# Kernel tuning notes

Hardware: AMD Instinct MI355X
Metric: run time of the kernel (lower is better)

## Reference

```python
import jax, jax.numpy as jnp
import numpy as np

N = 50000
E = 600000
D_IN = 128
D_HID = 128
D_OUT = 40
EPS = 1e-5


def glorot(key, shape):
    lim = float(np.sqrt(6.0 / (shape[0] + shape[1])))
    return jax.random.uniform(key, shape, jnp.float32, -lim, lim)


def setup_inputs() -> dict:
    key = jax.random.key(0)
    ks = jax.random.split(key, 8)
    return {
        "node_feat": jax.random.normal(ks[0], (N, D_IN), jnp.float32),
        "edge_src": jax.random.randint(ks[1], (E,), 0, N, jnp.int32),
        "edge_dst": jax.random.randint(ks[2], (E,), 0, N, jnp.int32),
        # input BatchNorm (bn_1)
        "bn0_g": jnp.ones((D_IN,), jnp.float32),
        "bn0_b": jnp.zeros((D_IN,), jnp.float32),
        # conv 1 (in -> hidden) + its BN
        "W1": glorot(ks[3], (D_IN, D_HID)),
        "b1": jnp.zeros((D_HID,), jnp.float32),
        "bn1_g": jnp.ones((D_HID,), jnp.float32),
        "bn1_b": jnp.zeros((D_HID,), jnp.float32),
        # conv 2 (hidden -> hidden) + its BN
        "W2": glorot(ks[4], (D_HID, D_HID)),
        "b2": jnp.zeros((D_HID,), jnp.float32),
        "bn2_g": jnp.ones((D_HID,), jnp.float32),
        "bn2_b": jnp.zeros((D_HID,), jnp.float32),
        # final projection
        "Wf": glorot(ks[5], (D_HID, D_OUT)),
        "bf": jnp.zeros((D_OUT,), jnp.float32),
    }


def batchnorm(x, gamma, beta):
    # BatchNorm1d over nodes (batch-stat / training-mode normalization)
    mu = jnp.mean(x, axis=0)
    var = jnp.mean(jnp.square(x - mu), axis=0)
    return gamma * (x - mu) * jax.lax.rsqrt(var + EPS) + beta


def gcn_conv(x, W, b, src, dst, norm, self_norm):
    # GCNConv: D^{-1/2}(A+I)D^{-1/2} X W + b
    h = x @ W  # [N, d_out]
    agg = jax.ops.segment_sum(h[src] * norm[:, None], dst, num_segments=N)
    agg = agg + h * self_norm[:, None]  # self-loop contribution
    return agg + b


def reference(node_feat, edge_src, edge_dst, bn0_g, bn0_b, W1, b1, bn1_g, bn1_b,
              W2, b2, bn2_g, bn2_b, Wf, bf):
    # degree with self-loops: deg_i = |{e : dst(e)=i}| + 1
    deg = jnp.ones((N,), jnp.float32).at[edge_dst].add(1.0)
    dinv = jax.lax.rsqrt(deg)
    norm = dinv[edge_src] * dinv[edge_dst]  # [E]
    self_norm = dinv * dinv                 # [N]

    x = batchnorm(node_feat, bn0_g, bn0_b)

    x = gcn_conv(x, W1, b1, edge_src, edge_dst, norm, self_norm)
    x = batchnorm(x, bn1_g, bn1_b)
    x = jax.nn.relu(x)  # dropout is identity in eval mode

    x = gcn_conv(x, W2, b2, edge_src, edge_dst, norm, self_norm)
    x = batchnorm(x, bn2_g, bn2_b)
    x = jax.nn.relu(x)

    return x @ Wf + bf  # [N, D_OUT]
```

## Files before the change

### kernel.cpp

```cpp
#include <hip/hip_runtime.h>
#include <cstdint>
#include <cstddef>


#define CS_BLOCKS 512

typedef short  s8v __attribute__((ext_vector_type(8)));
typedef ushort u8v __attribute__((ext_vector_type(8)));
typedef float  f4v __attribute__((ext_vector_type(4)));

__device__ inline ushort f2bf(float f) {
    uint u = __float_as_uint(f);
    return (ushort)((u + 0x7fffu + ((u >> 16) & 1u)) >> 16);
}
__device__ inline float bf2f(ushort u) {
    return __uint_as_float((uint)u << 16);
}
__device__ inline float2 bf2f2(uint u) {
    float2 r;
    r.x = __uint_as_float(u << 16);
    r.y = __uint_as_float(u & 0xffff0000u);
    return r;
}

__global__ __launch_bounds__(256) void k_prolog(const float* __restrict__ X,
                                                int n, float* __restrict__ part,
                                                const float* __restrict__ W1,
                                                const float* __restrict__ W2,
                                                ushort* __restrict__ Wswz,
                                                int* __restrict__ cnt) {
    const int bid = blockIdx.x;
    if (bid < CS_BLOCKS) {
        __shared__ float ls[8 * 128];
        __shared__ float lq[8 * 128];
        const int c4    = threadIdx.x & 31;
        const int rslot = threadIdx.x >> 5;
        float4 s4 = make_float4(0.f, 0.f, 0.f, 0.f);
        float4 q4 = make_float4(0.f, 0.f, 0.f, 0.f);
        const float4* X4 = (const float4*)X;
        for (int r = bid * 8 + rslot; r < n; r += CS_BLOCKS * 8) {
            float4 v = X4[(size_t)r * 32 + c4];
            s4.x += v.x; s4.y += v.y; s4.z += v.z; s4.w += v.w;
            q4.x = fmaf(v.x, v.x, q4.x); q4.y = fmaf(v.y, v.y, q4.y);
            q4.z = fmaf(v.z, v.z, q4.z); q4.w = fmaf(v.w, v.w, q4.w);
        }
        *(float4*)&ls[rslot * 128 + c4 * 4] = s4;
        *(float4*)&lq[rslot * 128 + c4 * 4] = q4;
        __syncthreads();
        float t = 0.f;
        if (threadIdx.x < 128) {
            int c = threadIdx.x;
            #pragma unroll
            for (int k = 0; k < 8; ++k) t += ls[k * 128 + c];
        } else {
            int c = threadIdx.x - 128;
            #pragma unroll
            for (int k = 0; k < 8; ++k) t += lq[k * 128 + c];
        }
        part[bid * 256 + threadIdx.x] = t;
    } else if (bid < CS_BLOCKS + 16) {
        const int wb = bid - CS_BLOCKS;
        const float* W = (wb < 8) ? W1 : W2;
        ushort* out = Wswz + (wb < 8 ? 0 : 16384);
        int t  = (wb & 7) * 256 + threadIdx.x;
        int l  = t & 63;
        int fi = t >> 6;
        int ks = fi & 3, ct = fi >> 2;
        int c  = ct * 16 + (l & 15);
        int k0 = ks * 32 + ((l >> 4) << 3);
        ushort o[8];
        #pragma unroll
        for (int j = 0; j < 8; ++j)
            o[j] = f2bf(W[(size_t)(k0 + j) * 128 + c]);
        ushort4* dst = (ushort4*)(out + (size_t)t * 8);
        dst[0] = make_ushort4(o[0], o[1], o[2], o[3]);
        dst[1] = make_ushort4(o[4], o[5], o[6], o[7]);
    } else {
        const int zb = bid - CS_BLOCKS - 16;
        const int nv = n >> 2;
        int4* c4p = (int4*)cnt;
        const int4 z = make_int4(0, 0, 0, 0);
        for (int i = zb * 256 + threadIdx.x; i < nv; i += 64 * 256)
            c4p[i] = z;
        int i = (nv << 2) + zb * 256 + threadIdx.x;
        if (i < n) cnt[i] = 0;
    }
}

__device__ inline void redA_body(const float* __restrict__ part,
                                 float* __restrict__ part2,
                                 int nrows, int b) {
    const int c = threadIdx.x;
    const int per = (nrows + 63) >> 6;
    const int r0 = b * per;
    const int r1 = min(r0 + per, nrows);
    float t0 = 0.f, t1 = 0.f;
    int r = r0;
    for (; r + 2 <= r1; r += 2) {
        t0 += part[(size_t)r * 256 + c];
        t1 += part[(size_t)(r + 1) * 256 + c];
    }
    if (r < r1) t0 += part[(size_t)r * 256 + c];
    part2[b * 256 + c] = t0 + t1;
}

__global__ __launch_bounds__(256) void k_redA(const float* __restrict__ part,
                                              float* __restrict__ part2,
                                              int nrows) {
    redA_body(part, part2, nrows, blockIdx.x);
}

__device__ inline void bn_inblock(const float* __restrict__ part2,
                                  const float* __restrict__ g,
                                  const float* __restrict__ be,
                                  float invn, float* __restrict__ tmp,
                                  float* __restrict__ abuf,
                                  float* __restrict__ bbuf) {
    const int tid = threadIdx.x;
    float t = 0.f;
    #pragma unroll 8
    for (int r = 0; r < 64; ++r) t += part2[r * 256 + tid];
    tmp[tid] = t;
    __syncthreads();
    if (tid < 128) {
        float mu  = tmp[tid] * invn;
        float var = tmp[tid + 128] * invn - mu * mu;
        float av  = g[tid] * rsqrtf(var + 1e-5f);
        abuf[tid] = av;
        bbuf[tid] = be[tid] - mu * av;
    }
    __syncthreads();
}

__global__ __launch_bounds__(256) void k_count(const int* __restrict__ dst, int e,
                                               int* __restrict__ cnt,
                                               int* __restrict__ rank) {
    int i = blockIdx.x * 256 + threadIdx.x;
    if (i < e) rank[i] = atomicAdd(&cnt[dst[i]], 1);
}

__global__ __launch_bounds__(1024) void k_scanA(const int* __restrict__ cnt, int n,
                                                int* __restrict__ rs, int* __restrict__ bsum) {
    __shared__ int tmp[1024];
    int t = threadIdx.x;
    int i = blockIdx.x * 1024 + t;
    int v = (i < n) ? cnt[i] : 0;
    tmp[t] = v;
    __syncthreads();
    for (int off = 1; off < 1024; off <<= 1) {
        int x = (t >= off) ? tmp[t - off] : 0;
        __syncthreads();
        tmp[t] += x;
        __syncthreads();
    }
    if (i < n) rs[i] = tmp[t] - v;
    if (t == 1023) bsum[blockIdx.x] = tmp[t];
}

__global__ __launch_bounds__(256) void k_scanC(int* __restrict__ rs,
                                               const int* __restrict__ bsum,
                                               const int* __restrict__ cnt,
                                               float* __restrict__ dinv,
                                               int n, int e) {
    __shared__ int base;
    int chunk = (int)(blockIdx.x >> 2);
    if (threadIdx.x == 0) {
        int s = 0;
        for (int c = 0; c < chunk; ++c) s += bsum[c];
        base = s;
    }
    __syncthreads();
    int i = blockIdx.x * 256 + threadIdx.x;
    if (i < n) {
        rs[i] += base;
        dinv[i] = rsqrtf((float)(cnt[i] + 1));
    }
    if (blockIdx.x == 0 && threadIdx.x == 0) rs[n] = e;
}

__global__ __launch_bounds__(256) void k_fill(const int* __restrict__ src,
                                              const int* __restrict__ dst, int e,
                                              const int* __restrict__ rs,
                                              const int* __restrict__ rank,
                                              const float* __restrict__ dinv,
                                              int2* __restrict__ ep,
                                              const float* __restrict__ part,
                                              float* __restrict__ part2,
                                              int fillBlocks) {
    const int bid = blockIdx.x;
    if (bid < fillBlocks) {
        int i = bid * 256 + threadIdx.x;
        if (i < e) {
            int d = dst[i], s = src[i];
            int p = rs[d] + rank[i];
            float nm = dinv[s] * dinv[d];
            ep[p] = make_int2(s, __float_as_int(nm));
        }
    } else {
        redA_body(part, part2, CS_BLOCKS, bid - fillBlocks);
    }
}

template<int BF16IN>
__global__ __launch_bounds__(256) void k_gemm_mfma(const void* __restrict__ Xv,
                                                   const ushort* __restrict__ Wswz,
                                                   const float* __restrict__ part2,
                                                   const float* __restrict__ g,
                                                   const float* __restrict__ be,
                                                   float invn, int relu,
                                                   ushort* __restrict__ H, int n) {
    __shared__ ushort xb[64 * 128];
    __shared__ float tmp[256];
    __shared__ float abuf[128], bbuf[128];
    const int tid  = threadIdx.x;
    const int row0 = blockIdx.x * 64;

    bn_inblock(part2, g, be, invn, tmp, abuf, bbuf);

    if (BF16IN) {
        const ushort* X = (const ushort*)Xv;
        for (int i = tid; i < 64 * 16; i += 256) {
            int r = i >> 4, c8 = i & 15;
            int gr = row0 + r;
            u8v raw = {0, 0, 0, 0, 0, 0, 0, 0};
            if (gr < n) raw = *(const u8v*)(X + (size_t)gr * 128 + c8 * 8);
            ushort o[8];
            #pragma unroll
            for (int j = 0; j < 8; ++j) {
                float f = fmaf(bf2f(raw[j]), abuf[c8 * 8 + j], bbuf[c8 * 8 + j]);
                if (relu) f = fmaxf(f, 0.f);
                o[j] = f2bf(f);
            }
            int off = (r * 256 + c8 * 16) ^ ((r & 7) << 4);
            ushort4* dst = (ushort4*)((char*)xb + off);
            dst[0] = make_ushort4(o[0], o[1], o[2], o[3]);
            dst[1] = make_ushort4(o[4], o[5], o[6], o[7]);
        }
    } else {
        const float* X = (const float*)Xv;
        for (int i = tid; i < 64 * 32; i += 256) {
            int r = i >> 5, c4 = i & 31;
            int gr = row0 + r;
            float4 v = make_float4(0.f, 0.f, 0.f, 0.f);
            if (gr < n) v = ((const float4*)X)[(size_t)gr * 32 + c4];
            float4 a4 = *(const float4*)&abuf[c4 * 4];
            float4 b4 = *(const float4*)&bbuf[c4 * 4];
            v.x = fmaf(v.x, a4.x, b4.x);
            v.y = fmaf(v.y, a4.y, b4.y);
            v.z = fmaf(v.z, a4.z, b4.z);
            v.w = fmaf(v.w, a4.w, b4.w);
            if (relu) {
                v.x = fmaxf(v.x, 0.f); v.y = fmaxf(v.y, 0.f);
                v.z = fmaxf(v.z, 0.f); v.w = fmaxf(v.w, 0.f);
            }
            ushort4 pk = make_ushort4(f2bf(v.x), f2bf(v.y), f2bf(v.z), f2bf(v.w));
            int off = (r * 256 + c4 * 8) ^ ((r & 7) << 4);
            *(ushort4*)((char*)xb + off) = pk;
        }
    }
    __syncthreads();

    const int wv = tid >> 6;
    const int l  = tid & 63;
    const int arow = wv * 16 + (l & 15);

    s8v afr[4];
    #pragma unroll
    for (int ks = 0; ks < 4; ++ks) {
        int off = (arow * 256 + ks * 64 + ((l >> 4) << 4)) ^ ((arow & 7) << 4);
        afr[ks] = *(const s8v*)((const char*)xb + off);
    }

    const s8v* wf = (const s8v*)Wswz;
    f4v acc[8];
    #pragma unroll
    for (int ct = 0; ct < 8; ++ct) {
        f4v c = {0.f, 0.f, 0.f, 0.f};
        #pragma unroll
        for (int ks = 0; ks < 4; ++ks) {
            s8v bb = wf[(ct * 4 + ks) * 64 + l];
            c = __builtin_amdgcn_mfma_f32_16x16x32_bf16(afr[ks], bb, c, 0, 0, 0);
        }
        acc[ct] = c;
    }

    const int rbase = row0 + wv * 16 + ((l >> 4) << 2);
    const int cidx  = l & 15;
    #pragma unroll
    for (int r = 0; r < 4; ++r) {
        int gr = rbase + r;
        if (gr < n) {
            #pragma unroll
            for (int ct = 0; ct < 8; ++ct)
                H[(size_t)gr * 128 + ct * 16 + cidx] = f2bf(acc[ct][r]);
        }
    }
}

template<int NP>
__device__ inline void quad_batch(const ushort* __restrict__ H,
                                  const int2* __restrict__ ep,
                                  int i, int q, int sl, float* __restrict__ a) {
    int2 p[NP]; uint4 v[NP];
    #pragma unroll
    for (int k = 0; k < NP; ++k) p[k] = ep[i + 4 * k + q];
    #pragma unroll
    for (int k = 0; k < NP; ++k)
        v[k] = ((const uint4*)(H + (size_t)p[k].x * 128))[sl];
    #pragma unroll
    for (int k = 0; k < NP; ++k) {
        float w = __int_as_float(p[k].y);
        float2 f0 = bf2f2(v[k].x), f1 = bf2f2(v[k].y);
        float2 f2 = bf2f2(v[k].z), f3 = bf2f2(v[k].w);
        a[0] = fmaf(w, f0.x, a[0]); a[1] = fmaf(w, f0.y, a[1]);
        a[2] = fmaf(w, f1.x, a[2]); a[3] = fmaf(w, f1.y, a[3]);
        a[4] = fmaf(w, f2.x, a[4]); a[5] = fmaf(w, f2.y, a[5]);
        a[6] = fmaf(w, f3.x, a[6]); a[7] = fmaf(w, f3.y, a[7]);
    }
}

__global__ __launch_bounds__(256) void k_aggregate(const ushort* __restrict__ H,
                                                   const int* __restrict__ rs,
                                                   const int2* __restrict__ ep,
                                                   const float* __restrict__ dinv,
                                                   ushort* __restrict__ AGG,
                                                   float* __restrict__ part, int n) {
    __shared__ float red[4][128];
    __shared__ float redq[4][128];
    const int wv   = threadIdx.x >> 6;
    const int lane = threadIdx.x & 63;
    const int q    = lane >> 4;
    const int sl   = lane & 15;
    const int node = blockIdx.x * 4 + wv;
    float a[8] = {0.f, 0.f, 0.f, 0.f, 0.f, 0.f, 0.f, 0.f};

    if (node < n) {
        if (q == 0) {
            float sn = dinv[node]; sn *= sn;
            uint4 sv = ((const uint4*)(H + (size_t)node * 128))[sl];
            float2 f0 = bf2f2(sv.x), f1 = bf2f2(sv.y);
            float2 f2 = bf2f2(sv.z), f3 = bf2f2(sv.w);
            a[0] = sn * f0.x; a[1] = sn * f0.y;
            a[2] = sn * f1.x; a[3] = sn * f1.y;
            a[4] = sn * f2.x; a[5] = sn * f2.y;
            a[6] = sn * f3.x; a[7] = sn * f3.y;
        }
        int i  = rs[node];
        int i1 = rs[node + 1];
        for (; i + 16 <= i1; i += 16) quad_batch<4>(H, ep, i, q, sl, a);
        if (i + 8 <= i1) { quad_batch<2>(H, ep, i, q, sl, a); i += 8; }
        if (i + 4 <= i1) { quad_batch<1>(H, ep, i, q, sl, a); i += 4; }
        if (i < i1) {
            int idx = min(i + q, i1 - 1);
            int2 p = ep[idx];
            float w = (i + q < i1) ? __int_as_float(p.y) : 0.f;
            uint4 v = ((const uint4*)(H + (size_t)p.x * 128))[sl];
            float2 f0 = bf2f2(v.x), f1 = bf2f2(v.y);
            float2 f2 = bf2f2(v.z), f3 = bf2f2(v.w);
            a[0] = fmaf(w, f0.x, a[0]); a[1] = fmaf(w, f0.y, a[1]);
            a[2] = fmaf(w, f1.x, a[2]); a[3] = fmaf(w, f1.y, a[3]);
            a[4] = fmaf(w, f2.x, a[4]); a[5] = fmaf(w, f2.y, a[5]);
            a[6] = fmaf(w, f3.x, a[6]); a[7] = fmaf(w, f3.y, a[7]);
        }
        #pragma unroll
        for (int j = 0; j < 8; ++j) {
            a[j] += __shfl_xor(a[j], 16);
            a[j] += __shfl_xor(a[j], 32);
        }
        if (q == 0) {
            u8v o;
            #pragma unroll
            for (int j = 0; j < 8; ++j) o[j] = f2bf(a[j]);
            *(u8v*)(AGG + (size_t)node * 128 + sl * 8) = o;
        }
    }

    if (q == 0) {
        *(float4*)&red[wv][8 * sl]      = make_float4(a[0], a[1], a[2], a[3]);
        *(float4*)&red[wv][8 * sl + 4]  = make_float4(a[4], a[5], a[6], a[7]);
        *(float4*)&redq[wv][8 * sl]     = make_float4(a[0] * a[0], a[1] * a[1],
                                                      a[2] * a[2], a[3] * a[3]);
        *(float4*)&redq[wv][8 * sl + 4] = make_float4(a[4] * a[4], a[5] * a[5],
                                                      a[6] * a[6], a[7] * a[7]);
    }
    __syncthreads();
    const int t = threadIdx.x;
    if (t < 128)
        part[(size_t)blockIdx.x * 256 + t] =
            red[0][t] + red[1][t] + red[2][t] + red[3][t];
    else {
        int c = t - 128;
        part[(size_t)blockIdx.x * 256 + t] =
            redq[0][c] + redq[1][c] + redq[2][c] + redq[3][c];
    }
}

__global__ __launch_bounds__(256) void k_gemm_out(const ushort* __restrict__ X,
                                                  const float* __restrict__ Wf,
                                                  const float* __restrict__ bfv,
                                                  const float* __restrict__ part2,
                                                  const float* __restrict__ g,
                                                  const float* __restrict__ be,
                                                  float invn,
                                                  float* __restrict__ OUT, int n) {
    __shared__ float xl[32 * 132];
    __shared__ float wt[40 * 132];
    __shared__ float tmp[256];
    __shared__ float abuf[128], bbuf[128];
    const int tid = threadIdx.x;

    bn_inblock(part2, g, be, invn, tmp, abuf, bbuf);

    for (int i = tid; i < 128 * 40; i += 256) {
        int c = i / 40;
        int j = i - c * 40;
        wt[j * 132 + c] = Wf[i];
    }
    const int row0 = blockIdx.x * 32;
    for (int i = tid; i < 32 * 16; i += 256) {
        int r = i >> 4, c8 = i & 15;
        int gr = row0 + r;
        u8v raw = {0, 0, 0, 0, 0, 0, 0, 0};
        if (gr < n) raw = *(const u8v*)(X + (size_t)gr * 128 + c8 * 8);
        float o[8];
        #pragma unroll
        for (int j = 0; j < 8; ++j)
            o[j] = fmaxf(fmaf(bf2f(raw[j]), abuf[c8 * 8 + j],
                              bbuf[c8 * 8 + j]), 0.f);
        *(float4*)&xl[r * 132 + c8 * 8]     = make_float4(o[0], o[1], o[2], o[3]);
        *(float4*)&xl[r * 132 + c8 * 8 + 4] = make_float4(o[4], o[5], o[6], o[7]);
    }
    __syncthreads();

    const int rg = tid >> 3;
    const int cg = tid & 7;
    const int j0 = cg * 5;
    float acc[5] = {0.f, 0.f, 0.f, 0.f, 0.f};
    for (int c = 0; c < 128; c += 4) {
        float4 xv = *(const float4*)&xl[rg * 132 + c];
        #pragma unroll
        for (int j = 0; j < 5; ++j) {
            float4 wv = *(const float4*)&wt[(j0 + j) * 132 + c];
            acc[j] = fmaf(xv.x, wv.x, acc[j]);
            acc[j] = fmaf(xv.y, wv.y, acc[j]);
            acc[j] = fmaf(xv.z, wv.z, acc[j]);
            acc[j] = fmaf(xv.w, wv.w, acc[j]);
        }
    }
    int gr = row0 + rg;
    if (gr < n) {
        #pragma unroll
        for (int j = 0; j < 5; ++j)
            OUT[(size_t)gr * 40 + j0 + j] = acc[j] + bfv[j0 + j];
    }
}

extern "C" void kernel_launch(void* const* d_in, const int* in_sizes, int n_in,
                              void* d_out, int out_size, void* d_ws, size_t ws_size,
                              hipStream_t stream) {
    const float* X0      = (const float*)d_in[0];
    const int*   edgesrc = (const int*)d_in[1];
    const int*   edgedst = (const int*)d_in[2];
    const float* bn0g = (const float*)d_in[3];
    const float* bn0b = (const float*)d_in[4];
    const float* W1   = (const float*)d_in[5];
    const float* bn1g = (const float*)d_in[7];
    const float* bn1b = (const float*)d_in[8];
    const float* W2   = (const float*)d_in[9];
    const float* bn2g = (const float*)d_in[11];
    const float* bn2b = (const float*)d_in[12];
    const float* Wf   = (const float*)d_in[13];
    const float* bfv  = (const float*)d_in[14];

    const int n = in_sizes[0] / 128;
    const int e = in_sizes[1];
    float* OUT = (float*)d_out;

    const int aggBlocks = (n + 3) / 4;

    ushort* H    = (ushort*)d_ws;
    ushort* AGGb = H + (size_t)n * 128;
    float*  dinv = (float*)(AGGb + (size_t)n * 128);
    int2*   ep   = (int2*)(dinv + n);
    ushort* Wswz = (ushort*)(ep + e);
    int*    cnt  = (int*)(Wswz + 2 * 16384);
    int*    rs   = cnt + n;
    int*    rank = rs + n + 1;
    int*    bsum = rank + e;
    float*  part = (float*)(bsum + 64);
    float* part2 = part + (size_t)aggBlocks * 256;

    const float invn = 1.f / (float)n;
    const int nb = (n + 1023) / 1024;
    const int fillBlocks = (e + 255) / 256;

    k_prolog<<<CS_BLOCKS + 16 + 64, 256, 0, stream>>>(X0, n, part, W1, W2,
                                                      Wswz, cnt);

    k_count<<<(e + 255) / 256, 256, 0, stream>>>(edgedst, e, cnt, rank);
    k_scanA<<<nb, 1024, 0, stream>>>(cnt, n, rs, bsum);
    k_scanC<<<(n + 255) / 256, 256, 0, stream>>>(rs, bsum, cnt, dinv, n, e);
    k_fill<<<fillBlocks + 64, 256, 0, stream>>>(edgesrc, edgedst, e, rs, rank,
                                                dinv, ep, part, part2,
                                                fillBlocks);

    const int gemmBlocks = (n + 63) / 64;

    k_gemm_mfma<0><<<gemmBlocks, 256, 0, stream>>>(X0, Wswz, part2, bn0g, bn0b,
                                                   invn, 0, H, n);
    k_aggregate<<<aggBlocks, 256, 0, stream>>>(H, rs, ep, dinv, AGGb, part, n);

    k_redA<<<64, 256, 0, stream>>>(part, part2, aggBlocks);
    k_gemm_mfma<1><<<gemmBlocks, 256, 0, stream>>>(AGGb, Wswz + 16384, part2,
                                                   bn1g, bn1b, invn, 1, H, n);
    k_aggregate<<<aggBlocks, 256, 0, stream>>>(H, rs, ep, dinv, AGGb, part, n);

    k_redA<<<64, 256, 0, stream>>>(part, part2, aggBlocks);
    k_gemm_out<<<(n + 31) / 32, 256, 0, stream>>>(AGGb, Wf, bfv, part2, bn2g,
                                                  bn2b, invn, OUT, n);
}
```

Before: 230.6 us.

## Merge edge fill into first GEMM launch and BN reduction into scan

The input-BatchNorm partial reduction moves from the fill kernel into extra blocks of the scan-finalize kernel. The CSR edge fill now runs as extra blocks of the first MFMA GEMM launch, since the two are independent. This removes one kernel launch and lets the edge scatter overlap with the GEMM. The aggregation tail also gains a 12-edge batch step to cut per-node remainder iterations. The heterogeneous blocks share one launch, so register and LDS use is set by the GEMM body, which may lower occupancy for the fill blocks.

```diff
diff --git a/kernel.cpp b/kernel.cpp
--- a/kernel.cpp
+++ b/kernel.cpp
@@ -161,59 +161,43 @@
                                                const int* __restrict__ bsum,
                                                const int* __restrict__ cnt,
                                                float* __restrict__ dinv,
-                                               int n, int e) {
+                                               int n, int e,
+                                               const float* __restrict__ part,
+                                               float* __restrict__ part2,
+                                               int scanBlocks) {
+    const int bid = blockIdx.x;
+    if (bid >= scanBlocks) {
+        redA_body(part, part2, CS_BLOCKS, bid - scanBlocks);
+        return;
+    }
     __shared__ int base;
-    int chunk = (int)(blockIdx.x >> 2);
+    int chunk = (int)(bid >> 2);
     if (threadIdx.x == 0) {
         int s = 0;
         for (int c = 0; c < chunk; ++c) s += bsum[c];
         base = s;
     }
     __syncthreads();
-    int i = blockIdx.x * 256 + threadIdx.x;
+    int i = bid * 256 + threadIdx.x;
     if (i < n) {
         rs[i] += base;
         dinv[i] = rsqrtf((float)(cnt[i] + 1));
     }
-    if (blockIdx.x == 0 && threadIdx.x == 0) rs[n] = e;
-}
-
-__global__ __launch_bounds__(256) void k_fill(const int* __restrict__ src,
-                                              const int* __restrict__ dst, int e,
-                                              const int* __restrict__ rs,
-                                              const int* __restrict__ rank,
-                                              const float* __restrict__ dinv,
-                                              int2* __restrict__ ep,
-                                              const float* __restrict__ part,
-                                              float* __restrict__ part2,
-                                              int fillBlocks) {
-    const int bid = blockIdx.x;
-    if (bid < fillBlocks) {
-        int i = bid * 256 + threadIdx.x;
-        if (i < e) {
-            int d = dst[i], s = src[i];
-            int p = rs[d] + rank[i];
-            float nm = dinv[s] * dinv[d];
-            ep[p] = make_int2(s, __float_as_int(nm));
-        }
-    } else {
-        redA_body(part, part2, CS_BLOCKS, bid - fillBlocks);
-    }
+    if (bid == 0 && threadIdx.x == 0) rs[n] = e;
 }
 
 template<int BF16IN>
-__global__ __launch_bounds__(256) void k_gemm_mfma(const void* __restrict__ Xv,
-                                                   const ushort* __restrict__ Wswz,
-                                                   const float* __restrict__ part2,
-                                                   const float* __restrict__ g,
-                                                   const float* __restrict__ be,
-                                                   float invn, int relu,
-                                                   ushort* __restrict__ H, int n) {
+__device__ inline void gemm_body(const void* __restrict__ Xv,
+                                 const ushort* __restrict__ Wswz,
+                                 const float* __restrict__ part2,
+                                 const float* __restrict__ g,
+                                 const float* __restrict__ be,
+                                 float invn, int relu,
+                                 ushort* __restrict__ H, int n, int row0) {
     __shared__ ushort xb[64 * 128];
     __shared__ float tmp[256];
     __shared__ float abuf[128], bbuf[128];
-    const int tid  = threadIdx.x;
-    const int row0 = blockIdx.x * 64;
+    const int tid = threadIdx.x;
 
     bn_inblock(part2, g, be, invn, tmp, abuf, bbuf);
 
@@ -297,6 +281,45 @@
     }
 }
 
+__global__ __launch_bounds__(256) void k_gemm_mfma(const ushort* __restrict__ X,
+                                                   const ushort* __restrict__ Wswz,
+                                                   const float* __restrict__ part2,
+                                                   const float* __restrict__ g,
+                                                   const float* __restrict__ be,
+                                                   float invn, int relu,
+                                                   ushort* __restrict__ H, int n) {
+    gemm_body<1>(X, Wswz, part2, g, be, invn, relu, H, n, blockIdx.x * 64);
+}
+
+__global__ __launch_bounds__(256) void k_gemm_fill(const float* __restrict__ X,
+                                                   const ushort* __restrict__ Wswz,
+                                                   const float* __restrict__ part2,
+                                                   const float* __restrict__ g,
+                                                   const float* __restrict__ be,
+                                                   float invn,
+                                                   ushort* __restrict__ H, int n,
+                                                   int gemmBlocks,
+                                                   const int* __restrict__ src,
+                                                   const int* __restrict__ dst,
+                                                   int e,
+                                                   const int* __restrict__ rs,
+                                                   const int* __restrict__ rank,
+                                                   const float* __restrict__ dinv,
+                                                   int2* __restrict__ ep) {
+    const int bid = blockIdx.x;
+    if (bid < gemmBlocks) {
+        gemm_body<0>(X, Wswz, part2, g, be, invn, 0, H, n, bid * 64);
+    } else {
+        int i = (bid - gemmBlocks) * 256 + threadIdx.x;
+        if (i < e) {
+            int d = dst[i], s = src[i];
+            int p = rs[d] + rank[i];
+            float nm = dinv[s] * dinv[d];
+            ep[p] = make_int2(s, __float_as_int(nm));
+        }
+    }
+}
+
 template<int NP>
 __device__ inline void quad_batch(const ushort* __restrict__ H,
                                   const int2* __restrict__ ep,
@@ -348,8 +371,9 @@
         int i  = rs[node];
         int i1 = rs[node + 1];
         for (; i + 16 <= i1; i += 16) quad_batch<4>(H, ep, i, q, sl, a);
-        if (i + 8 <= i1) { quad_batch<2>(H, ep, i, q, sl, a); i += 8; }
-        if (i + 4 <= i1) { quad_batch<1>(H, ep, i, q, sl, a); i += 4; }
+        if (i + 12 <= i1) { quad_batch<3>(H, ep, i, q, sl, a); i += 12; }
+        if (i + 8  <= i1) { quad_batch<2>(H, ep, i, q, sl, a); i += 8; }
+        if (i + 4  <= i1) { quad_batch<1>(H, ep, i, q, sl, a); i += 4; }
         if (i < i1) {
             int idx = min(i + q, i1 - 1);
             int2 p = ep[idx];
@@ -493,28 +517,23 @@
     const float invn = 1.f / (float)n;
     const int nb = (n + 1023) / 1024;
     const int fillBlocks = (e + 255) / 256;
+    const int scanBlocks = (n + 255) / 256;
+    const int gemmBlocks = (n + 63) / 64;
 
     k_prolog<<<CS_BLOCKS + 16 + 64, 256, 0, stream>>>(X0, n, part, W1, W2,
                                                       Wswz, cnt);
-
     k_count<<<(e + 255) / 256, 256, 0, stream>>>(edgedst, e, cnt, rank);
     k_scanA<<<nb, 1024, 0, stream>>>(cnt, n, rs, bsum);
-    k_scanC<<<(n + 255) / 256, 256, 0, stream>>>(rs, bsum, cnt, dinv, n, e);
-    k_fill<<<fillBlocks + 64, 256, 0, stream>>>(edgesrc, edgedst, e, rs, rank,
-                                                dinv, ep, part, part2,
-                                                fillBlocks);
-
-    const int gemmBlocks = (n + 63) / 64;
-
-    k_gemm_mfma<0><<<gemmBlocks, 256, 0, stream>>>(X0, Wswz, part2, bn0g, bn0b,
-                                                   invn, 0, H, n);
+    k_scanC<<<scanBlocks + 64, 256, 0, stream>>>(rs, bsum, cnt, dinv, n, e,
+                                                 part, part2, scanBlocks);
+    k_gemm_fill<<<gemmBlocks + fillBlocks, 256, 0, stream>>>(
+        X0, Wswz, part2, bn0g, bn0b, invn, H, n, gemmBlocks,
+        edgesrc, edgedst, e, rs, rank, dinv, ep);
     k_aggregate<<<aggBlocks, 256, 0, stream>>>(H, rs, ep, dinv, AGGb, part, n);
-
     k_redA<<<64, 256, 0, stream>>>(part, part2, aggBlocks);
-    k_gemm_mfma<1><<<gemmBlocks, 256, 0, stream>>>(AGGb, Wswz + 16384, part2,
-                                                   bn1g, bn1b, invn, 1, H, n);
+    k_gemm_mfma<<<gemmBlocks, 256, 0, stream>>>(AGGb, Wswz + 16384, part2,
+                                                bn1g, bn1b, invn, 1, H, n);
     k_aggregate<<<aggBlocks, 256, 0, stream>>>(H, rs, ep, dinv, AGGb, part, n);
-
     k_redA<<<64, 256, 0, stream>>>(part, part2, aggBlocks);
     k_gemm_out<<<(n + 31) / 32, 256, 0, stream>>>(AGGb, Wf, bfv, part2, bn2g,
                                                   bn2b, invn, OUT, n);
```

Result: faster. 218.8 us (-5.1%).
